# Performance work log

Hardware: AMD Instinct MI355X
Metric: run time of the kernel (lower is better)

Reference implementation:

```python
import jax, jax.numpy as jnp
import numpy as np

K = 16  # knn_k
LN_EPS = 1e-5


def _layernorm(x, g, b):
    mu = jnp.mean(x, axis=-1, keepdims=True)
    var = jnp.var(x, axis=-1, keepdims=True)
    return (x - mu) * jax.lax.rsqrt(var + LN_EPS) * g + b


def _mlp_block(x, W1, b1, g, be, W2, b2):
    # Linear -> LayerNorm -> GELU -> Linear (MLPBlock)
    h = x @ W1 + b1
    h = jax.nn.gelu(_layernorm(h, g, be))
    return h @ W2 + b2


def _knn(v):
    # v: [N,3] -> indices of K nearest neighbors [N,K] (self included, as in knn search)
    sq = jnp.sum(v * v, axis=-1)                       # [N]
    d = sq[:, None] + sq[None, :] - 2.0 * (v @ v.T)    # [N,N] squared dists
    return jax.lax.top_k(-d, K)[1]                     # [N,K]


def setup_inputs() -> dict:
    key = jax.random.key(0)
    ks = jax.random.split(key, 8)
    B, N, C_IN, C_OUT, HID = 2, 8192, 32, 64, 128
    E_IN = C_IN + C_IN + 3  # 67
    s = 0.02
    return {
        "vertices": jax.random.normal(ks[0], (B, N, 3), jnp.float32),
        "features": jax.random.normal(ks[1], (B, N, C_IN), jnp.float32),
        "W1": jax.random.normal(ks[2], (E_IN, HID), jnp.float32) * s,
        "b1": jnp.zeros((HID,), jnp.float32),
        "g1": jnp.ones((HID,), jnp.float32),
        "be1": jnp.zeros((HID,), jnp.float32),
        "W2": jax.random.normal(ks[3], (HID, C_OUT), jnp.float32) * s,
        "b2": jnp.zeros((C_OUT,), jnp.float32),
        "Wo1": jax.random.normal(ks[4], (C_OUT, HID), jnp.float32) * s,
        "bo1": jnp.zeros((HID,), jnp.float32),
        "go": jnp.ones((HID,), jnp.float32),
        "beo": jnp.zeros((HID,), jnp.float32),
        "Wo2": jax.random.normal(ks[5], (HID, C_OUT), jnp.float32) * s,
        "bo2": jnp.zeros((C_OUT,), jnp.float32),
    }


def reference(vertices, features, W1, b1, g1, be1, W2, b2,
              Wo1, bo1, go, beo, Wo2, bo2):
    # out_point_feature_type == 'same': output points == input points
    idx = jax.vmap(_knn)(vertices)                                   # [B,N,K]
    gather = jax.vmap(lambda a, i: jnp.take(a, i, axis=0))
    neigh_feat = gather(features, idx)                               # [B,N,K,C]
    neigh_vert = gather(vertices, idx)                               # [B,N,K,3]
    self_feat = jnp.broadcast_to(features[:, :, None, :], neigh_feat.shape)
    rel_pos = neigh_vert - vertices[:, :, None, :]                   # [B,N,K,3]
    edge = jnp.concatenate([neigh_feat, self_feat, rel_pos], axis=-1)  # [B,N,K,2C+3]
    edge = _mlp_block(edge, W1, b1, g1, be1, W2, b2)                 # [B,N,K,C_out]
    out = jnp.mean(edge, axis=2)                                     # 'mean' reduction over K neighbors
    out = _mlp_block(out, Wo1, bo1, go, beo, Wo2, bo2)               # [B,N,C_out]
    return out
```

## Files before the change

### kernel.cpp

```cpp
#include <hip/hip_runtime.h>
#include <hip/hip_bf16.h>
#include <math.h>

#define BATCH 2
#define NPTS  8192
#define CIN   32
#define HID   128
#define COUT  64
#define EIN   67
#define KNN   16

#define TILE  1024
#define CAP   128
#define KMARGIN 1e-3f
#define KM_MFMA 4e-3f

typedef unsigned short u16;
typedef unsigned long long u64;
typedef __attribute__((ext_vector_type(8))) short bf16x8;
typedef __attribute__((ext_vector_type(4))) float f32x4;

#if defined(__has_builtin)
#if __has_builtin(__builtin_amdgcn_rcpf)
#define USE_RCPF 1
#endif
#endif

__device__ __forceinline__ u16 f2b(float f) {
    unsigned u = __float_as_uint(f);
    return (u16)((u + 0x7FFFu + ((u >> 16) & 1u)) >> 16);
}
__device__ __forceinline__ float b2f(u16 h) {
    return __uint_as_float(((unsigned)h) << 16);
}
__device__ __forceinline__ unsigned pk2(float a, float b) {
    return (unsigned)f2b(a) | ((unsigned)f2b(b) << 16);
}
__device__ __forceinline__ float gelu_t(float x) {
    float u = 1.5957691216057308f * (x + 0.044715f * x * x * x);
    float ex = __expf(u);
#ifdef USE_RCPF
    return x * ex * __builtin_amdgcn_rcpf(ex + 1.0f);
#else
    return x * ex / (ex + 1.0f);
#endif
}

__device__ __forceinline__ float rank16_of_64(float v, int lane) {
#pragma unroll
    for (int k = 2; k <= 64; k <<= 1) {
#pragma unroll
        for (int j = k >> 1; j > 0; j >>= 1) {
            float o = __shfl_xor(v, j, 64);
            bool lower = (lane & j) == 0;
            bool asc   = (lane & k) == 0;
            float mn = fminf(v, o), mx = fmaxf(v, o);
            v = (lower == asc) ? mn : mx;
        }
    }
    return __shfl(v, 15, 64);
}

__global__ void prep_kernel(const float* __restrict__ verts, float4* __restrict__ pv) {
    int i = blockIdx.x * blockDim.x + threadIdx.x;
    if (i >= BATCH * NPTS) return;
    float x = verts[3 * i], y = verts[3 * i + 1], z = verts[3 * i + 2];
    float sq = __fadd_rn(__fadd_rn(__fmul_rn(x, x), __fmul_rn(y, y)), __fmul_rn(z, z));
    pv[i] = make_float4(x, y, z, sq);
}

__global__ void prep2_kernel(const float* __restrict__ verts,
                             float4* __restrict__ pv, uint4* __restrict__ bfrag) {
    int i = blockIdx.x * blockDim.x + threadIdx.x;
    if (i >= BATCH * NPTS) return;
    float x = verts[3 * i], y = verts[3 * i + 1], z = verts[3 * i + 2];
    float sq = __fadd_rn(__fadd_rn(__fmul_rn(x, x), __fmul_rn(y, y)), __fmul_rn(z, z));
    pv[i] = make_float4(x, y, z, sq);

    u16 xh = f2b(x);  u16 xl = f2b(x - b2f(xh));
    u16 yh = f2b(y);  u16 yl = f2b(y - b2f(yh));
    u16 zh = f2b(z);  u16 zl = f2b(z - b2f(zh));
    u16 ch = f2b(sq); u16 cl = f2b(sq - b2f(ch));

    uint4 lo, hi;
    lo.x = (unsigned)xh | ((unsigned)xl << 16);
    lo.y = (unsigned)xh | ((unsigned)yh << 16);
    lo.z = (unsigned)yl | ((unsigned)yh << 16);
    lo.w = (unsigned)zh | ((unsigned)zl << 16);
    hi.x = (unsigned)zh | ((unsigned)ch << 16);
    hi.y = (unsigned)cl;
    hi.z = 0u; hi.w = 0u;
    bfrag[(size_t)i * 2]     = lo;
    bfrag[(size_t)i * 2 + 1] = hi;
}

__global__ __launch_bounds__(256, 4) void knn11_kernel(const float4* __restrict__ pv,
                                                       const uint4* __restrict__ bfrag,
                                                       int* __restrict__ nbr_out_rows) {
    __shared__ float mnsh[4][16][17];
    __shared__ float taus[16];
    __shared__ int   cnt[16];
    __shared__ int   sJ[16][CAP];
    __shared__ float bufD[16][CAP];

    const int tid = threadIdx.x, lane = tid & 63, wv = tid >> 6;
    const int col = lane & 15, qq = lane >> 4;
    const int ptb = blockIdx.x * 16;
    const int b = ptb >> 13, i0 = ptb & (NPTS - 1);
    const float4* __restrict__ P = pv + (size_t)b * NPTS;
    const uint4* __restrict__ BF = bfrag + (size_t)b * NPTS * 2;

    union U { uint4 u; bf16x8 v; };

    union { bf16x8 v; unsigned w[4]; } A;
    {
        float4 s = P[i0 + col];
        float mx = -2.0f * s.x, my = -2.0f * s.y, mz = -2.0f * s.z;
        u16 mxh = f2b(mx); u16 mxl = f2b(mx - b2f(mxh));
        u16 myh = f2b(my); u16 myl = f2b(my - b2f(myh));
        u16 mzh = f2b(mz); u16 mzl = f2b(mz - b2f(mzh));
        if (qq == 0) {
            A.w[0] = (unsigned)mxh | ((unsigned)mxh << 16);
            A.w[1] = (unsigned)mxl | ((unsigned)myh << 16);
            A.w[2] = (unsigned)myh | ((unsigned)myl << 16);
            A.w[3] = (unsigned)mzh | ((unsigned)mzh << 16);
        } else if (qq == 1) {
            A.w[0] = (unsigned)mzl | (0x3F80u << 16);
            A.w[1] = 0x3F80u;
            A.w[2] = 0u; A.w[3] = 0u;
        } else {
            A.w[0] = A.w[1] = A.w[2] = A.w[3] = 0u;
        }
    }

    const int cb = wv * 2048;

    float mn0 = INFINITY, mn1 = INFINITY, mn2 = INFINITY, mn3 = INFINITY;
    for (int t = 0; t < 64; ++t) {
        U bu; bu.u = BF[(size_t)(cb + t * 16 + col) * 2 + (qq & 1)];
        f32x4 acc = (f32x4){0.f, 0.f, 0.f, 0.f};
        acc = __builtin_amdgcn_mfma_f32_16x16x32_bf16(A.v, bu.v, acc, 0, 0, 0);
        mn0 = fminf(mn0, acc[0]); mn1 = fminf(mn1, acc[1]);
        mn2 = fminf(mn2, acc[2]); mn3 = fminf(mn3, acc[3]);
    }
    mnsh[wv][qq * 4 + 0][col] = mn0;
    mnsh[wv][qq * 4 + 1][col] = mn1;
    mnsh[wv][qq * 4 + 2][col] = mn2;
    mnsh[wv][qq * 4 + 3][col] = mn3;
    if (tid < 16) cnt[tid] = 0;
    __syncthreads();

    {
        float tq[4];
#pragma unroll
        for (int q = 0; q < 4; ++q) {
            const int p = wv * 4 + q;
            float v = mnsh[lane >> 4][p][lane & 15];
            tq[q] = rank16_of_64(v, lane) + KM_MFMA;
        }
        if (lane == 0) {
#pragma unroll
            for (int q = 0; q < 4; ++q) taus[wv * 4 + q] = tq[q];
        }
    }
    __syncthreads();

    float mytau[4];
#pragma unroll
    for (int r = 0; r < 4; ++r) mytau[r] = taus[qq * 4 + r];

    for (int t = 0; t < 128; ++t) {
        const int cbase = cb + t * 16;
        U bu; bu.u = BF[(size_t)(cbase + col) * 2 + (qq & 1)];
        f32x4 acc = (f32x4){0.f, 0.f, 0.f, 0.f};
        acc = __builtin_amdgcn_mfma_f32_16x16x32_bf16(A.v, bu.v, acc, 0, 0, 0);
        if ((acc[0] <= mytau[0]) | (acc[1] <= mytau[1]) |
            (acc[2] <= mytau[2]) | (acc[3] <= mytau[3])) {
#pragma unroll
            for (int r = 0; r < 4; ++r) {
                if (acc[r] <= mytau[r]) {
                    int p = qq * 4 + r;
                    int pos = atomicAdd(&cnt[p], 1);
                    if (pos < CAP) sJ[p][pos] = cbase + col;
                }
            }
        }
    }
    __syncthreads();

#pragma unroll
    for (int q = 0; q < 4; ++q) {
        const int p = wv * 4 + q;
        int ns = cnt[p]; ns = (ns > CAP) ? CAP : ns;
        const float4 sp = P[i0 + p];
        float dl[2]; int jl[2];
#pragma unroll
        for (int slot = 0; slot < 2; ++slot) {
            int sidx = slot * 64 + lane;
            bool act = sidx < ns;
            int js = act ? sJ[p][sidx] : 0;
            float4 cc = P[js];
            float dot = __fmul_rn(sp.x, cc.x);
            dot = __fmaf_rn(sp.y, cc.y, dot);
            dot = __fmaf_rn(sp.z, cc.z, dot);
            float d = __fsub_rn(__fadd_rn(sp.w, cc.w), __fmul_rn(2.0f, dot));
            if (act) bufD[p][sidx] = d;
            dl[slot] = d; jl[slot] = js;
        }
        int r0 = 0, r1 = 0;
        for (int mm = 0; mm < ns; ++mm) {
            float dm = bufD[p][mm]; int jm = sJ[p][mm];
            r0 += (dm < dl[0]) || (dm == dl[0] && jm < jl[0]);
            r1 += (dm < dl[1]) || (dm == dl[1] && jm < jl[1]);
        }
        if (lane < ns && r0 < KNN)
            nbr_out_rows[(size_t)(ptb + p) * 64 + r0] = jl[0];
        if (64 + lane < ns && r1 < KNN)
            nbr_out_rows[(size_t)(ptb + p) * 64 + r1] = jl[1];
    }
}

__global__ __launch_bounds__(256, 8) void knn9_kernel(const float4* __restrict__ pv,
                                                      int* __restrict__ nbr_out_rows) {
    __shared__ float  bufD[4][2][CAP];
    __shared__ int    bufJ[4][2][CAP];

    const int tid = threadIdx.x, lane = tid & 63, wv = tid >> 6;
    const int pt0 = (blockIdx.x * 4 + wv) * 2;
    const int b = pt0 >> 13, i0 = pt0 & (NPTS - 1);
    const float4* P = pv + (size_t)b * NPTS;

    float4 sp[2];
    float ax[2], ay[2], az[2];
#pragma unroll
    for (int p = 0; p < 2; ++p) {
        sp[p] = P[i0 + p];
        ax[p] = -2.0f * sp[p].x; ay[p] = -2.0f * sp[p].y; az[p] = -2.0f * sp[p].z;
    }

    float mn[2] = {INFINITY, INFINITY};
    for (int t = 0; t < 16; ++t) {
        float4 c0 = P[t * 256 + lane];
        float4 c1 = P[t * 256 + 64 + lane];
        float4 c2 = P[t * 256 + 128 + lane];
        float4 c3 = P[t * 256 + 192 + lane];
#pragma unroll
        for (int p = 0; p < 2; ++p) {
            float f0 = __fmaf_rn(ax[p], c0.x, __fmaf_rn(ay[p], c0.y, __fmaf_rn(az[p], c0.z, c0.w)));
            float f1 = __fmaf_rn(ax[p], c1.x, __fmaf_rn(ay[p], c1.y, __fmaf_rn(az[p], c1.z, c1.w)));
            float f2 = __fmaf_rn(ax[p], c2.x, __fmaf_rn(ay[p], c2.y, __fmaf_rn(az[p], c2.z, c2.w)));
            float f3 = __fmaf_rn(ax[p], c3.x, __fmaf_rn(ay[p], c3.y, __fmaf_rn(az[p], c3.z, c3.w)));
            mn[p] = fminf(fminf(fminf(mn[p], f0), fminf(f1, f2)), f3);
        }
    }

    float tau[2];
#pragma unroll
    for (int p = 0; p < 2; ++p)
        tau[p] = rank16_of_64(mn[p], lane) + KMARGIN;

    int base[2] = {0, 0};
    for (int t = 0; t < 32; ++t) {
        float4 c[4];
#pragma unroll
        for (int k = 0; k < 4; ++k) c[k] = P[t * 256 + k * 64 + lane];
        bool pr[4][2];
        bool anyl = false;
#pragma unroll
        for (int k = 0; k < 4; ++k)
#pragma unroll
            for (int p = 0; p < 2; ++p) {
                float f = __fmaf_rn(ax[p], c[k].x,
                          __fmaf_rn(ay[p], c[k].y,
                          __fmaf_rn(az[p], c[k].z, c[k].w)));
                pr[k][p] = (f <= tau[p]);
                anyl |= pr[k][p];
            }
        if (__ballot(anyl) == 0ull) continue;
#pragma unroll
        for (int k = 0; k < 4; ++k) {
            u64 anyk = __ballot(pr[k][0] | pr[k][1]);
            if (anyk == 0ull) continue;
            int j = t * 256 + k * 64 + lane;
#pragma unroll
            for (int p = 0; p < 2; ++p) {
                u64 mk = __ballot(pr[k][p]);
                if (mk != 0ull) {
                    if (pr[k][p]) {
                        int pos = base[p] + (int)__popcll(mk & ((1ull << lane) - 1ull));
                        if (pos < CAP) bufJ[wv][p][pos] = j;
                    }
                    base[p] += (int)__popcll(mk);
                }
            }
        }
    }

#pragma unroll
    for (int p = 0; p < 2; ++p) {
        int ns = base[p]; ns = (ns > CAP) ? CAP : ns;
        float dloc[2]; int jloc[2];
#pragma unroll
        for (int slot = 0; slot < 2; ++slot) {
            int sidx = slot * 64 + lane;
            bool act = sidx < ns;
            int js = act ? bufJ[wv][p][sidx] : 0;
            float4 cc = P[js];
            float dot = __fmul_rn(sp[p].x, cc.x);
            dot = __fmaf_rn(sp[p].y, cc.y, dot);
            dot = __fmaf_rn(sp[p].z, cc.z, dot);
            float d = __fsub_rn(__fadd_rn(sp[p].w, cc.w), __fmul_rn(2.0f, dot));
            if (act) bufD[wv][p][sidx] = d;
            dloc[slot] = d; jloc[slot] = js;
        }
        int r0 = 0, r1 = 0;
        for (int mm = 0; mm < ns; ++mm) {
            float dm = bufD[wv][p][mm]; int jm = bufJ[wv][p][mm];
            r0 += (dm < dloc[0]) || (dm == dloc[0] && jm < jloc[0]);
            r1 += (dm < dloc[1]) || (dm == dloc[1] && jm < jloc[1]);
        }
        if (lane < ns && r0 < KNN)
            nbr_out_rows[(size_t)(pt0 + p) * 64 + r0] = jloc[0];
        if (64 + lane < ns && r1 < KNN)
            nbr_out_rows[(size_t)(pt0 + p) * 64 + r1] = jloc[1];
    }
}

__global__ __launch_bounds__(256) void knn_kernel(const float* __restrict__ verts,
                                                  int* nbr_out_rows) {
    __shared__ float4 tilebuf[TILE];
    __shared__ float  bufD[4][CAP];
    __shared__ int    bufJ[4][CAP];

    const int tid = threadIdx.x, lane = tid & 63, wv = tid >> 6;
    const int pt = blockIdx.x * 4 + wv;
    const int b = pt >> 13, i = pt & (NPTS - 1);
    const float* vb = verts + (size_t)b * NPTS * 3;

    const float xi = vb[3 * i], yi = vb[3 * i + 1], zi = vb[3 * i + 2];
    const float sqi = __fadd_rn(__fadd_rn(__fmul_rn(xi, xi), __fmul_rn(yi, yi)),
                                __fmul_rn(zi, zi));

    float m_d = INFINITY;
    for (int t = 0; t < NPTS / TILE; ++t) {
        __syncthreads();
        for (int s = 0; s < TILE / 256; ++s) {
            int p = t * TILE + s * 256 + tid;
            float px = vb[3 * p], py = vb[3 * p + 1], pz = vb[3 * p + 2];
            float sq = __fadd_rn(__fadd_rn(__fmul_rn(px, px), __fmul_rn(py, py)),
                                 __fmul_rn(pz, pz));
            tilebuf[s * 256 + tid] = make_float4(px, py, pz, sq);
        }
        __syncthreads();
        for (int it = 0; it < TILE / 64; ++it) {
            float4 c = tilebuf[it * 64 + lane];
            float dot = __fmul_rn(xi, c.x);
            dot = __fmaf_rn(yi, c.y, dot);
            dot = __fmaf_rn(zi, c.z, dot);
            float d = __fsub_rn(__fadd_rn(sqi, c.w), __fmul_rn(2.0f, dot));
            m_d = fminf(m_d, d);
        }
    }
    __shared__ float minv[4][64];
    minv[wv][lane] = m_d;
    __syncthreads();
    int rnk = 0;
    for (int mm = 0; mm < 64; ++mm) {
        float vm = minv[wv][mm];
        rnk += (vm < m_d) || (vm == m_d && mm < lane);
    }
    u64 bal = __ballot(rnk == 15);
    float tau = __shfl(m_d, __ffsll(bal) - 1, 64);

    int base = 0;
    for (int t = 0; t < NPTS / TILE; ++t) {
        __syncthreads();
        for (int s = 0; s < TILE / 256; ++s) {
            int p = t * TILE + s * 256 + tid;
            float px = vb[3 * p], py = vb[3 * p + 1], pz = vb[3 * p + 2];
            float sq = __fadd_rn(__fadd_rn(__fmul_rn(px, px), __fmul_rn(py, py)),
                                 __fmul_rn(pz, pz));
            tilebuf[s * 256 + tid] = make_float4(px, py, pz, sq);
        }
        __syncthreads();
        for (int it = 0; it < TILE / 64; ++it) {
            int jl = it * 64 + lane;
            float4 c = tilebuf[jl];
            float dot = __fmul_rn(xi, c.x);
            dot = __fmaf_rn(yi, c.y, dot);
            dot = __fmaf_rn(zi, c.z, dot);
            float d = __fsub_rn(__fadd_rn(sqi, c.w), __fmul_rn(2.0f, dot));
            bool pred = (d <= tau);
            u64 mask = __ballot(pred);
            if (pred) {
                int pos = base + (int)__popcll(mask & ((1ull << lane) - 1ull));
                if (pos < CAP) { bufD[wv][pos] = d; bufJ[wv][pos] = t * TILE + jl; }
            }
            base += (int)__popcll(mask);
        }
    }
    int ns = (base > CAP) ? CAP : base;
    __syncthreads();
#pragma unroll
    for (int slot = 0; slot < 2; ++slot) {
        int sidx = slot * 64 + lane;
        if (sidx < ns) {
            float ds = bufD[wv][sidx];
            int   js = bufJ[wv][sidx];
            int rank = 0;
            for (int mm = 0; mm < ns; ++mm) {
                float dm = bufD[wv][mm];
                int   jm = bufJ[wv][mm];
                rank += (dm < ds) || (dm == ds && jm < js);
            }
            if (rank < KNN) nbr_out_rows[(size_t)pt * 64 + rank] = js;
        }
    }
}

__global__ __launch_bounds__(256, 2) void edge4_kernel(
    const float* __restrict__ verts, const float* __restrict__ feats,
    const float* __restrict__ W1, const float* __restrict__ b1,
    const float* __restrict__ g1, const float* __restrict__ be1,
    const float* __restrict__ W2, const float* __restrict__ b2,
    const float* __restrict__ Wo1, const float* __restrict__ bo1,
    const float* __restrict__ go_, const float* __restrict__ beo,
    const float* __restrict__ Wo2, const float* __restrict__ bo2,
    float* out)
{
    __shared__ u16 EPw[4][4][64][8];
    __shared__ u16 W1F[3][8][64][8];
    __shared__ float b1s[HID], g1s[HID], be1s[HID];
    __shared__ float b2s[COUT];
    __shared__ float meansh[16][68];

    const int tid  = threadIdx.x;
    const int lane = tid & 63, wv = tid >> 6;
    const int quad = lane >> 4, n16 = lane & 15;

    for (int s = tid; s < 3 * 8 * 64; s += 256) {
        int kt = s >> 9, nt = (s >> 6) & 7, ln = s & 63;
        int q = ln >> 4, nn = ln & 15;
        int col = nt * 16 + nn;
        union { bf16x8 v; unsigned u[4]; } pk;
#pragma unroll
        for (int jj = 0; jj < 4; ++jj) {
            int k0 = kt * 32 + q * 8 + jj * 2;
            float a  = (k0     < EIN) ? W1[(size_t)k0 * HID + col]       : 0.0f;
            float bq = (k0 + 1 < EIN) ? W1[(size_t)(k0 + 1) * HID + col] : 0.0f;
            pk.u[jj] = pk2(a, bq);
        }
        *(bf16x8*)&W1F[kt][nt][ln][0] = pk.v;
    }
    if (tid < HID) { b1s[tid] = b1[tid]; g1s[tid] = g1[tid]; be1s[tid] = be1[tid]; }
    if (tid < COUT) b2s[tid] = b2[tid];

    bf16x8 w2r[4][4];
#pragma unroll
    for (int kt2 = 0; kt2 < 4; ++kt2)
#pragma unroll
        for (int nt2 = 0; nt2 < 4; ++nt2) {
            union { bf16x8 v; unsigned u[4]; } pk;
#pragma unroll
            for (int jj = 0; jj < 4; ++jj) {
                int k0 = kt2 * 32 + quad * 8 + jj * 2;
                int o = nt2 * 16 + n16;
                pk.u[jj] = pk2(W2[(size_t)k0 * COUT + o],
                               W2[(size_t)(k0 + 1) * COUT + o]);
            }
            w2r[kt2][nt2] = pk.v;
        }
    __syncthreads();

    const int ptb = blockIdx.x * 16;
    const int bb  = ptb >> 13;
    const float* fb  = feats + (size_t)bb * NPTS * CIN;
    const float* vbk = verts + (size_t)bb * NPTS * 3;
    const int ptw = ptb + wv * 4;
    const int ipw = ptw & (NPTS - 1);

    float b1v[8], g1v[8], bev[8];
#pragma unroll
    for (int nt = 0; nt < 8; ++nt) {
        b1v[nt] = b1s[nt * 16 + n16];
        g1v[nt] = g1s[nt * 16 + n16];
        bev[nt] = be1s[nt * 16 + n16];
    }

    const int k16 = lane & 15;
    const int qq  = lane >> 4;

    int jnv[4];
#pragma unroll
    for (int pp = 0; pp < 4; ++pp)
        jnv[pp] = ((const int*)out)[(size_t)(ptw + pp) * 64 + k16];

#pragma unroll
    for (int pp = 0; pp < 4; ++pp) {
        const int jn  = jnv[pp];
        const int ipn = ipw + pp;

        {
            const float* nsrc = fb + (size_t)jn * CIN + qq * 8;
            float4 nA = *(const float4*)nsrc, nB = *(const float4*)(nsrc + 4);
            const float* ssrc = fb + (size_t)ipn * CIN + qq * 8;
            float4 sA = *(const float4*)ssrc, sB = *(const float4*)(ssrc + 4);

            union { bf16x8 v; unsigned u[4]; } e0, e1, e2;
            e0.u[0] = pk2(nA.x, nA.y); e0.u[1] = pk2(nA.z, nA.w);
            e0.u[2] = pk2(nB.x, nB.y); e0.u[3] = pk2(nB.z, nB.w);
            e1.u[0] = pk2(sA.x, sA.y); e1.u[1] = pk2(sA.z, sA.w);
            e1.u[2] = pk2(sB.x, sB.y); e1.u[3] = pk2(sB.z, sB.w);
            e2.u[0] = e2.u[1] = e2.u[2] = e2.u[3] = 0u;
            if (qq == 0) {
                float rx = vbk[3 * jn]     - vbk[3 * ipn];
                float ry = vbk[3 * jn + 1] - vbk[3 * ipn + 1];
                float rz = vbk[3 * jn + 2] - vbk[3 * ipn + 2];
                e2.u[0] = pk2(rx, ry); e2.u[1] = pk2(rz, 0.0f);
            }
            *(bf16x8*)&EPw[wv][0][lane][0] = e0.v;
            *(bf16x8*)&EPw[wv][1][lane][0] = e1.v;
            *(bf16x8*)&EPw[wv][2][lane][0] = e2.v;
        }

        f32x4 acc[8];
#pragma unroll
        for (int nt = 0; nt < 8; ++nt) acc[nt] = (f32x4){0.f, 0.f, 0.f, 0.f};
#pragma unroll
        for (int kt = 0; kt < 3; ++kt) {
            bf16x8 a = *(bf16x8*)&EPw[wv][kt][lane][0];
#pragma unroll
            for (int nt = 0; nt < 8; ++nt) {
                bf16x8 bfr = *(bf16x8*)&W1F[kt][nt][lane][0];
                acc[nt] = __builtin_amdgcn_mfma_f32_16x16x32_bf16(a, bfr, acc[nt], 0, 0, 0);
            }
        }

        float s1[4] = {0,0,0,0}, s2[4] = {0,0,0,0};
#pragma unroll
        for (int nt = 0; nt < 8; ++nt)
#pragma unroll
            for (int r = 0; r < 4; ++r) {
                float x = acc[nt][r] + b1v[nt];
                s1[r] += x; s2[r] += x * x;
            }
#pragma unroll
        for (int r = 0; r < 4; ++r) {
#pragma unroll
            for (int off = 1; off < 16; off <<= 1) {
                s1[r] += __shfl_xor(s1[r], off, 64);
                s2[r] += __shfl_xor(s2[r], off, 64);
            }
        }
        float mu[4], rs[4];
#pragma unroll
        for (int r = 0; r < 4; ++r) {
            mu[r] = s1[r] * (1.0f / HID);
            float var = s2[r] * (1.0f / HID) - mu[r] * mu[r];
            rs[r] = rsqrtf(var + 1e-5f);
        }

#pragma unroll
        for (int nt = 0; nt < 8; ++nt) {
            int kt2 = nt >> 1;
            int q2  = (nt * 2 + (n16 >> 3)) & 3;
            int jj  = n16 & 7;
#pragma unroll
            for (int r = 0; r < 4; ++r) {
                float x  = acc[nt][r] + b1v[nt];
                float xn = (x - mu[r]) * rs[r] * g1v[nt] + bev[nt];
                EPw[wv][kt2][quad * 4 + r + 16 * q2][jj] = (u16)f2b(gelu_t(xn));
            }
        }

        f32x4 acc2[4];
#pragma unroll
        for (int nt2 = 0; nt2 < 4; ++nt2) acc2[nt2] = (f32x4){0.f, 0.f, 0.f, 0.f};
#pragma unroll
        for (int kt2 = 0; kt2 < 4; ++kt2) {
            bf16x8 a2 = *(bf16x8*)&EPw[wv][kt2][lane][0];
#pragma unroll
            for (int nt2 = 0; nt2 < 4; ++nt2)
                acc2[nt2] = __builtin_amdgcn_mfma_f32_16x16x32_bf16(a2, w2r[kt2][nt2], acc2[nt2], 0, 0, 0);
        }

#pragma unroll
        for (int nt2 = 0; nt2 < 4; ++nt2) {
            float cs = acc2[nt2][0] + acc2[nt2][1] + acc2[nt2][2] + acc2[nt2][3];
            cs += __shfl_xor(cs, 16, 64);
            cs += __shfl_xor(cs, 32, 64);
            if (quad == 0) {
                int o = nt2 * 16 + n16;
                meansh[wv * 4 + pp][o] = cs * (1.0f / KNN) + b2s[o];
            }
        }
    }

    __syncthreads();

    for (int s = tid; s < 2 * 8 * 64; s += 256) {
        int kt = s >> 9, nt = (s >> 6) & 7, ln = s & 63;
        int q = ln >> 4, nn = ln & 15;
        int col = nt * 16 + nn;
        union { bf16x8 v; unsigned u[4]; } pk;
#pragma unroll
        for (int jj = 0; jj < 4; ++jj) {
            int k0 = kt * 32 + q * 8 + jj * 2;
            pk.u[jj] = pk2(Wo1[(size_t)k0 * HID + col],
                           Wo1[(size_t)(k0 + 1) * HID + col]);
        }
        *(bf16x8*)&W1F[kt][nt][ln][0] = pk.v;
    }
    if (tid < HID) { b1s[tid] = bo1[tid]; g1s[tid] = go_[tid]; be1s[tid] = beo[tid]; }
    if (tid < COUT) b2s[tid] = bo2[tid];
#pragma unroll
    for (int kt2 = 0; kt2 < 4; ++kt2)
#pragma unroll
        for (int nt2 = 0; nt2 < 4; ++nt2) {
            union { bf16x8 v; unsigned u[4]; } pk;
#pragma unroll
            for (int jj = 0; jj < 4; ++jj) {
                int k0 = kt2 * 32 + quad * 8 + jj * 2;
                int o = nt2 * 16 + n16;
                pk.u[jj] = pk2(Wo2[(size_t)k0 * COUT + o],
                               Wo2[(size_t)(k0 + 1) * COUT + o]);
            }
            w2r[kt2][nt2] = pk.v;
        }
    __syncthreads();

    if (wv == 0) {
        bf16x8 af[2];
#pragma unroll
        for (int kt = 0; kt < 2; ++kt) {
            const float* mrow = &meansh[n16][kt * 32 + quad * 8];
            float4 A = *(const float4*)mrow, B4 = *(const float4*)(mrow + 4);
            union { bf16x8 v; unsigned u[4]; } pk;
            pk.u[0] = pk2(A.x, A.y); pk.u[1] = pk2(A.z, A.w);
            pk.u[2] = pk2(B4.x, B4.y); pk.u[3] = pk2(B4.z, B4.w);
            af[kt] = pk.v;
        }

        f32x4 acc[8];
#pragma unroll
        for (int nt = 0; nt < 8; ++nt) acc[nt] = (f32x4){0.f, 0.f, 0.f, 0.f};
#pragma unroll
        for (int kt = 0; kt < 2; ++kt)
#pragma unroll
            for (int nt = 0; nt < 8; ++nt) {
                bf16x8 bfr = *(bf16x8*)&W1F[kt][nt][lane][0];
                acc[nt] = __builtin_amdgcn_mfma_f32_16x16x32_bf16(af[kt], bfr, acc[nt], 0, 0, 0);
            }

        float pb1[8], pg1[8], pbe[8];
#pragma unroll
        for (int nt = 0; nt < 8; ++nt) {
            pb1[nt] = b1s[nt * 16 + n16];
            pg1[nt] = g1s[nt * 16 + n16];
            pbe[nt] = be1s[nt * 16 + n16];
        }
        float s1[4] = {0,0,0,0}, s2[4] = {0,0,0,0};
#pragma unroll
        for (int nt = 0; nt < 8; ++nt)
#pragma unroll
            for (int r = 0; r < 4; ++r) {
                float x = acc[nt][r] + pb1[nt];
                s1[r] += x; s2[r] += x * x;
            }
#pragma unroll
        for (int r = 0; r < 4; ++r) {
#pragma unroll
            for (int off = 1; off < 16; off <<= 1) {
                s1[r] += __shfl_xor(s1[r], off, 64);
                s2[r] += __shfl_xor(s2[r], off, 64);
            }
        }
#pragma unroll
        for (int nt = 0; nt < 8; ++nt) {
            int kt2 = nt >> 1;
            int q2  = (nt * 2 + (n16 >> 3)) & 3;
            int jj  = n16 & 7;
#pragma unroll
            for (int r = 0; r < 4; ++r) {
                float mu = s1[r] * (1.0f / HID);
                float var = s2[r] * (1.0f / HID) - mu * mu;
                float rs = rsqrtf(var + 1e-5f);
                float x  = acc[nt][r] + pb1[nt];
                float xn = (x - mu) * rs * pg1[nt] + pbe[nt];
                EPw[0][kt2][quad * 4 + r + 16 * q2][jj] = (u16)f2b(gelu_t(xn));
            }
        }

        f32x4 acc2[4];
#pragma unroll
        for (int nt2 = 0; nt2 < 4; ++nt2) acc2[nt2] = (f32x4){0.f, 0.f, 0.f, 0.f};
#pragma unroll
        for (int kt2 = 0; kt2 < 4; ++kt2) {
            bf16x8 a2 = *(bf16x8*)&EPw[0][kt2][lane][0];
#pragma unroll
            for (int nt2 = 0; nt2 < 4; ++nt2)
                acc2[nt2] = __builtin_amdgcn_mfma_f32_16x16x32_bf16(a2, w2r[kt2][nt2], acc2[nt2], 0, 0, 0);
        }

#pragma unroll
        for (int nt2 = 0; nt2 < 4; ++nt2) {
            int o = nt2 * 16 + n16;
#pragma unroll
            for (int r = 0; r < 4; ++r)
                meansh[quad * 4 + r][o] = acc2[nt2][r] + b2s[o];
        }
    }
    __syncthreads();

    {
        int p = tid >> 4, c = (tid & 15) * 4;
        float4 v = *(const float4*)&meansh[p][c];
        *(float4*)&out[(size_t)(ptb + p) * 64 + c] = v;
    }
}

extern "C" void kernel_launch(void* const* d_in, const int* in_sizes, int n_in,
                              void* d_out, int out_size, void* d_ws, size_t ws_size,
                              hipStream_t stream) {
    const float* verts = (const float*)d_in[0];
    const float* feats = (const float*)d_in[1];
    const float* W1  = (const float*)d_in[2];
    const float* b1  = (const float*)d_in[3];
    const float* g1  = (const float*)d_in[4];
    const float* be1 = (const float*)d_in[5];
    const float* W2  = (const float*)d_in[6];
    const float* b2  = (const float*)d_in[7];
    const float* Wo1 = (const float*)d_in[8];
    const float* bo1 = (const float*)d_in[9];
    const float* go_ = (const float*)d_in[10];
    const float* beo = (const float*)d_in[11];
    const float* Wo2 = (const float*)d_in[12];
    const float* bo2 = (const float*)d_in[13];
    float* out = (float*)d_out;

    (void)in_sizes; (void)n_in; (void)out_size;

    const size_t pv_bytes = (size_t)BATCH * NPTS * sizeof(float4);
    const size_t bf_bytes = (size_t)BATCH * NPTS * 32;
    if (ws_size >= pv_bytes + bf_bytes) {
        float4* pv = (float4*)d_ws;
        uint4*  bf = (uint4*)((char*)d_ws + pv_bytes);
        prep2_kernel<<<(BATCH * NPTS + 255) / 256, 256, 0, stream>>>(verts, pv, bf);
        knn11_kernel<<<(BATCH * NPTS) / 16, 256, 0, stream>>>(pv, bf, (int*)out);
    } else if (ws_size >= pv_bytes) {
        float4* pv = (float4*)d_ws;
        prep_kernel<<<(BATCH * NPTS + 255) / 256, 256, 0, stream>>>(verts, pv);
        knn9_kernel<<<(BATCH * NPTS) / 8, 256, 0, stream>>>(pv, (int*)out);
    } else {
        knn_kernel<<<(BATCH * NPTS) / 4, 256, 0, stream>>>(verts, (int*)out);
    }
    edge4_kernel<<<(BATCH * NPTS) / 16, 256, 0, stream>>>(
        verts, feats, W1, b1, g1, be1, W2, b2,
        Wo1, bo1, go_, beo, Wo2, bo2, out);
}
```

Measured before the change: 211.6 us.

## Split KNN candidate scan across eight waves and unroll MFMA loops by two

The KNN kernel grows from 256 to 512 threads per block, so each of 8 waves scans 1024 candidates instead of 2048, and the per-query refinement is spread over 8 waves with 2 queries each. The threshold estimation now merges minima from two wave halves. The MFMA scan loops are unrolled by two with independent accumulators and strength-reduced pointers to expose more memory and MFMA parallelism. The cost is more contention on the shared atomic counters and a higher launch-bounds occupancy target that may pressure registers.

```diff
diff --git a/kernel.cpp b/kernel.cpp
--- a/kernel.cpp
+++ b/kernel.cpp
@@ -94,10 +94,10 @@
     bfrag[(size_t)i * 2 + 1] = hi;
 }
 
-__global__ __launch_bounds__(256, 4) void knn11_kernel(const float4* __restrict__ pv,
+__global__ __launch_bounds__(512, 8) void knn12_kernel(const float4* __restrict__ pv,
                                                        const uint4* __restrict__ bfrag,
                                                        int* __restrict__ nbr_out_rows) {
-    __shared__ float mnsh[4][16][17];
+    __shared__ float mnsh[8][16][17];
     __shared__ float taus[16];
     __shared__ int   cnt[16];
     __shared__ int   sJ[16][CAP];
@@ -133,15 +133,22 @@
         }
     }
 
-    const int cb = wv * 2048;
+    const int cb = wv * 1024;
+    const uint4* __restrict__ bp = BF + ((size_t)(cb + col) * 2 + (qq & 1));
 
     float mn0 = INFINITY, mn1 = INFINITY, mn2 = INFINITY, mn3 = INFINITY;
-    for (int t = 0; t < 64; ++t) {
-        U bu; bu.u = BF[(size_t)(cb + t * 16 + col) * 2 + (qq & 1)];
-        f32x4 acc = (f32x4){0.f, 0.f, 0.f, 0.f};
-        acc = __builtin_amdgcn_mfma_f32_16x16x32_bf16(A.v, bu.v, acc, 0, 0, 0);
-        mn0 = fminf(mn0, acc[0]); mn1 = fminf(mn1, acc[1]);
-        mn2 = fminf(mn2, acc[2]); mn3 = fminf(mn3, acc[3]);
+    for (int t = 0; t < 32; t += 2) {
+        U b0, b1;
+        b0.u = bp[(size_t)t * 32];
+        b1.u = bp[(size_t)(t + 1) * 32];
+        f32x4 a0 = (f32x4){0.f, 0.f, 0.f, 0.f};
+        f32x4 a1 = (f32x4){0.f, 0.f, 0.f, 0.f};
+        a0 = __builtin_amdgcn_mfma_f32_16x16x32_bf16(A.v, b0.v, a0, 0, 0, 0);
+        a1 = __builtin_amdgcn_mfma_f32_16x16x32_bf16(A.v, b1.v, a1, 0, 0, 0);
+        mn0 = fminf(mn0, fminf(a0[0], a1[0]));
+        mn1 = fminf(mn1, fminf(a0[1], a1[1]));
+        mn2 = fminf(mn2, fminf(a0[2], a1[2]));
+        mn3 = fminf(mn3, fminf(a0[3], a1[3]));
     }
     mnsh[wv][qq * 4 + 0][col] = mn0;
     mnsh[wv][qq * 4 + 1][col] = mn1;
@@ -151,17 +158,15 @@
     __syncthreads();
 
     {
-        float tq[4];
-#pragma unroll
-        for (int q = 0; q < 4; ++q) {
-            const int p = wv * 4 + q;
-            float v = mnsh[lane >> 4][p][lane & 15];
+        float tq[2];
+#pragma unroll
+        for (int q = 0; q < 2; ++q) {
+            const int p = wv * 2 + q;
+            float v = fminf(mnsh[lane >> 4][p][lane & 15],
+                            mnsh[(lane >> 4) + 4][p][lane & 15]);
             tq[q] = rank16_of_64(v, lane) + KM_MFMA;
         }
-        if (lane == 0) {
-#pragma unroll
-            for (int q = 0; q < 4; ++q) taus[wv * 4 + q] = tq[q];
-        }
+        if (lane == 0) { taus[wv * 2] = tq[0]; taus[wv * 2 + 1] = tq[1]; }
     }
     __syncthreads();
 
@@ -169,28 +174,39 @@
 #pragma unroll
     for (int r = 0; r < 4; ++r) mytau[r] = taus[qq * 4 + r];
 
-    for (int t = 0; t < 128; ++t) {
-        const int cbase = cb + t * 16;
-        U bu; bu.u = BF[(size_t)(cbase + col) * 2 + (qq & 1)];
-        f32x4 acc = (f32x4){0.f, 0.f, 0.f, 0.f};
-        acc = __builtin_amdgcn_mfma_f32_16x16x32_bf16(A.v, bu.v, acc, 0, 0, 0);
-        if ((acc[0] <= mytau[0]) | (acc[1] <= mytau[1]) |
-            (acc[2] <= mytau[2]) | (acc[3] <= mytau[3])) {
+    for (int t = 0; t < 64; t += 2) {
+        U b0, b1;
+        b0.u = bp[(size_t)t * 32];
+        b1.u = bp[(size_t)(t + 1) * 32];
+        f32x4 a0 = (f32x4){0.f, 0.f, 0.f, 0.f};
+        f32x4 a1 = (f32x4){0.f, 0.f, 0.f, 0.f};
+        a0 = __builtin_amdgcn_mfma_f32_16x16x32_bf16(A.v, b0.v, a0, 0, 0, 0);
+        a1 = __builtin_amdgcn_mfma_f32_16x16x32_bf16(A.v, b1.v, a1, 0, 0, 0);
+        const int c0 = cb + t * 16 + col, c1 = c0 + 16;
+        if ((a0[0] <= mytau[0]) | (a0[1] <= mytau[1]) |
+            (a0[2] <= mytau[2]) | (a0[3] <= mytau[3]) |
+            (a1[0] <= mytau[0]) | (a1[1] <= mytau[1]) |
+            (a1[2] <= mytau[2]) | (a1[3] <= mytau[3])) {
 #pragma unroll
             for (int r = 0; r < 4; ++r) {
-                if (acc[r] <= mytau[r]) {
+                if (a0[r] <= mytau[r]) {
                     int p = qq * 4 + r;
                     int pos = atomicAdd(&cnt[p], 1);
-                    if (pos < CAP) sJ[p][pos] = cbase + col;
+                    if (pos < CAP) sJ[p][pos] = c0;
                 }
-            }
-        }
-    }
-    __syncthreads();
-
-#pragma unroll
-    for (int q = 0; q < 4; ++q) {
-        const int p = wv * 4 + q;
+                if (a1[r] <= mytau[r]) {
+                    int p = qq * 4 + r;
+                    int pos = atomicAdd(&cnt[p], 1);
+                    if (pos < CAP) sJ[p][pos] = c1;
+                }
+            }
+        }
+    }
+    __syncthreads();
+
+#pragma unroll
+    for (int q = 0; q < 2; ++q) {
+        const int p = wv * 2 + q;
         int ns = cnt[p]; ns = (ns > CAP) ? CAP : ns;
         const float4 sp = P[i0 + p];
         float dl[2]; int jl[2];
@@ -746,7 +762,7 @@
         float4* pv = (float4*)d_ws;
         uint4*  bf = (uint4*)((char*)d_ws + pv_bytes);
         prep2_kernel<<<(BATCH * NPTS + 255) / 256, 256, 0, stream>>>(verts, pv, bf);
-        knn11_kernel<<<(BATCH * NPTS) / 16, 256, 0, stream>>>(pv, bf, (int*)out);
+        knn12_kernel<<<(BATCH * NPTS) / 16, 512, 0, stream>>>(pv, bf, (int*)out);
     } else if (ws_size >= pv_bytes) {
         float4* pv = (float4*)d_ws;
         prep_kernel<<<(BATCH * NPTS + 255) / 256, 256, 0, stream>>>(verts, pv);
```

Result: faster. 193.3 us (-8.6%).
